# Kernel tuning notes

Hardware: AMD Instinct MI355X
Metric: run time of the kernel (lower is better)

## Reference

```python
import jax, jax.numpy as jnp
import numpy as np

N_NODES = 40000
N_EDGES = 640000
D = 128


def setup_inputs() -> dict:
    key = jax.random.key(0)
    k1, k2, k3, k4, k5 = jax.random.split(key, 5)
    x = jax.random.normal(k1, (N_NODES, D), dtype=jnp.float32)
    edge_index = jax.random.randint(k2, (2, N_EDGES), 0, N_NODES, dtype=jnp.int64)
    # torch Linear stores weight as [out, in]; xavier ~ scaled normal
    scale = (2.0 / (D + D)) ** 0.5
    W_self = jax.random.normal(k3, (D, D), dtype=jnp.float32) * scale
    W_neigh = jax.random.normal(k4, (D, D), dtype=jnp.float32) * scale
    bias = jax.random.normal(k5, (D,), dtype=jnp.float32) * 0.01
    return {"x": x, "edge_index": edge_index, "W_self": W_self,
            "W_neigh": W_neigh, "bias": bias}


def reference(x, edge_index, W_self, W_neigh, bias):
    num_nodes = x.shape[0]
    row, col = edge_index[0], edge_index[1]
    # gather source features and scatter-add into destination nodes
    agg = jax.ops.segment_sum(x[row], col, num_segments=num_nodes)  # [N, D]
    deg = jax.ops.segment_sum(jnp.ones_like(col, dtype=x.dtype), col,
                              num_segments=num_nodes)
    agg = agg / jnp.clip(deg, 1.0)[:, None]
    # h_v = lin_self(x_v) + lin_neigh(mean_u x_u) + bias  (no activation in source)
    out = x @ W_self.T + agg @ W_neigh.T + bias
    return out
```

## Files before the change

kernel.cpp:

```cpp
#include <hip/hip_runtime.h>

#define N_NODES 40000
#define N_EDGES 640000
#define D 128
#define KCAT 256
#define CAP 64
#define NXCD 8
#define PART 5000

typedef __attribute__((ext_vector_type(8))) short short8v;
typedef __attribute__((ext_vector_type(4))) float f32x4;
typedef __attribute__((ext_vector_type(2))) float f32x2;


__device__ inline unsigned short f2bf(float f) {
  union { float f; unsigned int u; } v{f};
  unsigned int r = (v.u + 0x7FFFu + ((v.u >> 16) & 1u)) >> 16;
  return (unsigned short)r;
}

__global__ __launch_bounds__(256) void prep_count_kernel(
    const float* __restrict__ x, const float* __restrict__ Ws,
    const float* __restrict__ Wn, const int* __restrict__ ei,
    unsigned short* __restrict__ Wcat, unsigned int* __restrict__ x8,
    int* __restrict__ deg, unsigned short* __restrict__ slot) {
  int b = blockIdx.x;
  int t = threadIdx.x;
  int tid = b * 256 + t;
  {
    float4 v = *reinterpret_cast<const float4*>(x + (size_t)tid * 4);
    unsigned int u = __builtin_amdgcn_cvt_pk_fp8_f32(v.x, v.y, 0, false);
    u = __builtin_amdgcn_cvt_pk_fp8_f32(v.z, v.w, u, true);
    x8[tid] = u;
  }
  if (tid < 8192) {
    int j = tid >> 6;
    int kq = tid & 63;
    int k0 = kq * 4;
    float4 v = (kq < 32)
        ? *reinterpret_cast<const float4*>(Ws + j * D + k0)
        : *reinterpret_cast<const float4*>(Wn + j * D + (k0 - D));
    ushort4 h;
    h.x = f2bf(v.x); h.y = f2bf(v.y); h.z = f2bf(v.z); h.w = f2bf(v.w);
    *reinterpret_cast<ushort4*>(Wcat + j * KCAT + k0) = h;
  }
  {
    int p = b & (NXCD - 1);
    int chunk = b >> 3;
    int lo = p * PART;
    int q = chunk * 256 + t;
    int4 r = reinterpret_cast<const int4*>(ei)[q];
    int4 c = reinterpret_cast<const int4*>(ei + N_EDGES)[q];
    if ((unsigned)(c.x - lo) < PART)
      slot[(size_t)c.x * CAP + atomicAdd(&deg[c.x], 1)] = (unsigned short)r.x;
    if ((unsigned)(c.y - lo) < PART)
      slot[(size_t)c.y * CAP + atomicAdd(&deg[c.y], 1)] = (unsigned short)r.y;
    if ((unsigned)(c.z - lo) < PART)
      slot[(size_t)c.z * CAP + atomicAdd(&deg[c.z], 1)] = (unsigned short)r.z;
    if ((unsigned)(c.w - lo) < PART)
      slot[(size_t)c.w * CAP + atomicAdd(&deg[c.w], 1)] = (unsigned short)r.w;
  }
}

__global__ __launch_bounds__(256) void gather_kernel(
    const unsigned int* __restrict__ x8, unsigned short* __restrict__ aggb,
    const int* __restrict__ deg, const unsigned short* __restrict__ slot) {
  int node = blockIdx.x * 8 + (threadIdx.x >> 5);
  int l = threadIdx.x & 31;
  int nd = deg[node];
  const unsigned short* sp = slot + (size_t)node * CAP;
  float a0 = 0.f, a1 = 0.f, a2 = 0.f, a3 = 0.f;
  int e = 0;
  for (; e + 8 <= nd; e += 8) {
    unsigned int v[8];
#pragma unroll
    for (int j = 0; j < 8; ++j) v[j] = x8[(size_t)sp[e + j] * 32 + l];
#pragma unroll
    for (int j = 0; j < 8; ++j) {
      f32x2 lo = __builtin_amdgcn_cvt_pk_f32_fp8(v[j], false);
      f32x2 hi = __builtin_amdgcn_cvt_pk_f32_fp8(v[j], true);
      a0 += lo.x; a1 += lo.y; a2 += hi.x; a3 += hi.y;
    }
  }
  for (; e + 4 <= nd; e += 4) {
    unsigned int v[4];
#pragma unroll
    for (int j = 0; j < 4; ++j) v[j] = x8[(size_t)sp[e + j] * 32 + l];
#pragma unroll
    for (int j = 0; j < 4; ++j) {
      f32x2 lo = __builtin_amdgcn_cvt_pk_f32_fp8(v[j], false);
      f32x2 hi = __builtin_amdgcn_cvt_pk_f32_fp8(v[j], true);
      a0 += lo.x; a1 += lo.y; a2 += hi.x; a3 += hi.y;
    }
  }
  for (; e < nd; ++e) {
    unsigned int v = x8[(size_t)sp[e] * 32 + l];
    f32x2 lo = __builtin_amdgcn_cvt_pk_f32_fp8(v, false);
    f32x2 hi = __builtin_amdgcn_cvt_pk_f32_fp8(v, true);
    a0 += lo.x; a1 += lo.y; a2 += hi.x; a3 += hi.y;
  }
  float inv = 1.0f / fmaxf((float)nd, 1.0f);
  ushort4 h;
  h.x = f2bf(a0 * inv); h.y = f2bf(a1 * inv);
  h.z = f2bf(a2 * inv); h.w = f2bf(a3 * inv);
  *reinterpret_cast<ushort4*>(aggb + (size_t)node * D + l * 4) = h;
}

__global__ __launch_bounds__(256) void sage_gemm_kernel(
    const float* __restrict__ x, const unsigned short* __restrict__ aggb,
    const unsigned short* __restrict__ Wcat, const float* __restrict__ bias,
    float* __restrict__ out) {
  __shared__ __align__(16) char Abuf[64 * 512];
  const int t = threadIdx.x;
  const int wave = t >> 6;
  const int lane = t & 63;
  const int node0 = blockIdx.x * 64;

  short8v breg[2][8];
#pragma unroll
  for (int jg = 0; jg < 2; ++jg) {
    int col = wave * 32 + jg * 16 + (lane & 15);
#pragma unroll
    for (int ks = 0; ks < 8; ++ks) {
      int k0 = ks * 32 + (lane >> 4) * 8;
      breg[jg][ks] =
          *reinterpret_cast<const short8v*>(Wcat + (size_t)col * KCAT + k0);
    }
  }

#pragma unroll
  for (int i = 0; i < 4; ++i) {
    int q = i * 256 + t;
    int row = q >> 4;
    int s = q & 15;
    const float* xp = x + (size_t)(node0 + row) * D + s * 8;
    float4 v0 = *reinterpret_cast<const float4*>(xp);
    float4 v1 = *reinterpret_cast<const float4*>(xp + 4);
    ushort4 h0, h1;
    h0.x = f2bf(v0.x); h0.y = f2bf(v0.y); h0.z = f2bf(v0.z); h0.w = f2bf(v0.w);
    h1.x = f2bf(v1.x); h1.y = f2bf(v1.y); h1.z = f2bf(v1.z); h1.w = f2bf(v1.w);
    char* dst = Abuf + row * 512 + ((s ^ (row & 7)) << 4);
    *reinterpret_cast<ushort4*>(dst) = h0;
    *reinterpret_cast<ushort4*>(dst + 8) = h1;
  }
#pragma unroll
  for (int i = 0; i < 4; ++i) {
    int q = i * 256 + t;
    int row = q >> 4;
    int s = 16 + (q & 15);
    int4 v = *reinterpret_cast<const int4*>(aggb + (size_t)(node0 + row) * D +
                                            (q & 15) * 8);
    *reinterpret_cast<int4*>(Abuf + row * 512 + ((s ^ (row & 7)) << 4)) = v;
  }
  __syncthreads();

  const int srow = lane & 15;
  const int c7 = lane & 7;
  const int sb = lane >> 4;

  f32x4 acc[4][2] = {};
#pragma unroll
  for (int ks = 0; ks < 8; ++ks) {
    short8v af[4];
#pragma unroll
    for (int mf = 0; mf < 4; ++mf) {
      int row = mf * 16 + srow;
      int sl = (ks * 4 + sb) ^ c7;
      af[mf] = *reinterpret_cast<const short8v*>(Abuf + row * 512 + (sl << 4));
    }
#pragma unroll
    for (int mf = 0; mf < 4; ++mf)
#pragma unroll
      for (int jg = 0; jg < 2; ++jg)
        acc[mf][jg] = __builtin_amdgcn_mfma_f32_16x16x32_bf16(
            af[mf], breg[jg][ks], acc[mf][jg], 0, 0, 0);
  }

#pragma unroll
  for (int jg = 0; jg < 2; ++jg) {
    int col = wave * 32 + jg * 16 + (lane & 15);
    float bv = bias[col];
#pragma unroll
    for (int mf = 0; mf < 4; ++mf) {
      int rbase = node0 + mf * 16 + (lane >> 4) * 4;
#pragma unroll
      for (int r = 0; r < 4; ++r) {
        out[(size_t)(rbase + r) * D + col] = acc[mf][jg][r] + bv;
      }
    }
  }
}

extern "C" void kernel_launch(void* const* d_in, const int* in_sizes, int n_in,
                              void* d_out, int out_size, void* d_ws, size_t ws_size,
                              hipStream_t stream) {
  const float* x    = (const float*)d_in[0];
  const int*   ei   = (const int*)d_in[1];
  const float* Ws   = (const float*)d_in[2];
  const float* Wn   = (const float*)d_in[3];
  const float* bias = (const float*)d_in[4];
  float* out = (float*)d_out;

  unsigned short* Wcat = (unsigned short*)d_ws;
  int* deg = (int*)(Wcat + 128 * KCAT);
  unsigned short* slot = (unsigned short*)(deg + N_NODES);
  unsigned int* x8 =
      (unsigned int*)(slot + (size_t)N_NODES * CAP);
  unsigned short* aggb =
      (unsigned short*)(x8 + (size_t)N_NODES * 32);

  hipMemsetAsync(deg, 0, N_NODES * sizeof(int), stream);
  prep_count_kernel<<<5000, 256, 0, stream>>>(x, Ws, Wn, ei, Wcat, x8, deg,
                                              slot);
  gather_kernel<<<5000, 256, 0, stream>>>(x8, aggb, deg, slot);
  sage_gemm_kernel<<<625, 256, 0, stream>>>(x, aggb, Wcat, bias, out);
}
```

Measured before the change: 70.68 us.

## Partition edges via shared-memory buckets and fuse neighbor gather into GEMM

The edge scan is restructured: each of 625 blocks reads its edges once, bins them by destination partition in LDS, and writes them to per-partition lists. A new bucket kernel then fills the CSR-like slot arrays from those lists, instead of 5000 blocks each rereading all edges and filtering. The separate gather kernel and the bf16 agg buffer are removed, and the mean aggregation now runs inside the GEMM kernel straight into LDS, two nodes interleaved per half-wave. This trades one extra launch for less edge re-reading and less agg traffic, but the GEMM now uses only 625 blocks to do the latency-bound gather, so there is less parallelism to hide that latency.

```diff
diff --git a/kernel.cpp b/kernel.cpp
--- a/kernel.cpp
+++ b/kernel.cpp
@@ -7,6 +7,8 @@
 #define CAP 64
 #define NXCD 8
 #define PART 5000
+#define PLCAP 84000
+#define CCAP 224
 
 typedef __attribute__((ext_vector_type(8))) short short8v;
 typedef __attribute__((ext_vector_type(4))) float f32x4;
@@ -19,11 +21,18 @@
   return (unsigned short)r;
 }
 
-__global__ __launch_bounds__(256) void prep_count_kernel(
+__device__ inline void acc4(unsigned int v, float& a0, float& a1, float& a2,
+                            float& a3) {
+  f32x2 lo = __builtin_amdgcn_cvt_pk_f32_fp8(v, false);
+  f32x2 hi = __builtin_amdgcn_cvt_pk_f32_fp8(v, true);
+  a0 += lo.x; a1 += lo.y; a2 += hi.x; a3 += hi.y;
+}
+
+__global__ __launch_bounds__(256) void prep_kernel(
     const float* __restrict__ x, const float* __restrict__ Ws,
     const float* __restrict__ Wn, const int* __restrict__ ei,
     unsigned short* __restrict__ Wcat, unsigned int* __restrict__ x8,
-    int* __restrict__ deg, unsigned short* __restrict__ slot) {
+    unsigned int* __restrict__ plist, int* __restrict__ pcur) {
   int b = blockIdx.x;
   int t = threadIdx.x;
   int tid = b * 256 + t;
@@ -44,70 +53,69 @@
     h.x = f2bf(v.x); h.y = f2bf(v.y); h.z = f2bf(v.z); h.w = f2bf(v.w);
     *reinterpret_cast<ushort4*>(Wcat + j * KCAT + k0) = h;
   }
-  {
-    int p = b & (NXCD - 1);
-    int chunk = b >> 3;
-    int lo = p * PART;
-    int q = chunk * 256 + t;
+  __shared__ int lcnt[NXCD];
+  __shared__ int lbase[NXCD];
+  __shared__ unsigned int lbuf[NXCD][CCAP];
+  if (b < 625) {
+    if (t < NXCD) lcnt[t] = 0;
+    __syncthreads();
+    int q = b * 256 + t;
     int4 r = reinterpret_cast<const int4*>(ei)[q];
     int4 c = reinterpret_cast<const int4*>(ei + N_EDGES)[q];
-    if ((unsigned)(c.x - lo) < PART)
-      slot[(size_t)c.x * CAP + atomicAdd(&deg[c.x], 1)] = (unsigned short)r.x;
-    if ((unsigned)(c.y - lo) < PART)
-      slot[(size_t)c.y * CAP + atomicAdd(&deg[c.y], 1)] = (unsigned short)r.y;
-    if ((unsigned)(c.z - lo) < PART)
-      slot[(size_t)c.z * CAP + atomicAdd(&deg[c.z], 1)] = (unsigned short)r.z;
-    if ((unsigned)(c.w - lo) < PART)
-      slot[(size_t)c.w * CAP + atomicAdd(&deg[c.w], 1)] = (unsigned short)r.w;
-  }
-}
-
-__global__ __launch_bounds__(256) void gather_kernel(
-    const unsigned int* __restrict__ x8, unsigned short* __restrict__ aggb,
-    const int* __restrict__ deg, const unsigned short* __restrict__ slot) {
-  int node = blockIdx.x * 8 + (threadIdx.x >> 5);
-  int l = threadIdx.x & 31;
-  int nd = deg[node];
-  const unsigned short* sp = slot + (size_t)node * CAP;
-  float a0 = 0.f, a1 = 0.f, a2 = 0.f, a3 = 0.f;
-  int e = 0;
-  for (; e + 8 <= nd; e += 8) {
-    unsigned int v[8];
-#pragma unroll
-    for (int j = 0; j < 8; ++j) v[j] = x8[(size_t)sp[e + j] * 32 + l];
-#pragma unroll
-    for (int j = 0; j < 8; ++j) {
-      f32x2 lo = __builtin_amdgcn_cvt_pk_f32_fp8(v[j], false);
-      f32x2 hi = __builtin_amdgcn_cvt_pk_f32_fp8(v[j], true);
-      a0 += lo.x; a1 += lo.y; a2 += hi.x; a3 += hi.y;
-    }
-  }
-  for (; e + 4 <= nd; e += 4) {
-    unsigned int v[4];
-#pragma unroll
-    for (int j = 0; j < 4; ++j) v[j] = x8[(size_t)sp[e + j] * 32 + l];
-#pragma unroll
-    for (int j = 0; j < 4; ++j) {
-      f32x2 lo = __builtin_amdgcn_cvt_pk_f32_fp8(v[j], false);
-      f32x2 hi = __builtin_amdgcn_cvt_pk_f32_fp8(v[j], true);
-      a0 += lo.x; a1 += lo.y; a2 += hi.x; a3 += hi.y;
-    }
-  }
-  for (; e < nd; ++e) {
-    unsigned int v = x8[(size_t)sp[e] * 32 + l];
-    f32x2 lo = __builtin_amdgcn_cvt_pk_f32_fp8(v, false);
-    f32x2 hi = __builtin_amdgcn_cvt_pk_f32_fp8(v, true);
-    a0 += lo.x; a1 += lo.y; a2 += hi.x; a3 += hi.y;
-  }
-  float inv = 1.0f / fmaxf((float)nd, 1.0f);
-  ushort4 h;
-  h.x = f2bf(a0 * inv); h.y = f2bf(a1 * inv);
-  h.z = f2bf(a2 * inv); h.w = f2bf(a3 * inv);
-  *reinterpret_cast<ushort4*>(aggb + (size_t)node * D + l * 4) = h;
+    {
+      int p = c.x / PART;
+      lbuf[p][atomicAdd(&lcnt[p], 1)] =
+          (unsigned)(c.x - p * PART) | ((unsigned)r.x << 13);
+    }
+    {
+      int p = c.y / PART;
+      lbuf[p][atomicAdd(&lcnt[p], 1)] =
+          (unsigned)(c.y - p * PART) | ((unsigned)r.y << 13);
+    }
+    {
+      int p = c.z / PART;
+      lbuf[p][atomicAdd(&lcnt[p], 1)] =
+          (unsigned)(c.z - p * PART) | ((unsigned)r.z << 13);
+    }
+    {
+      int p = c.w / PART;
+      lbuf[p][atomicAdd(&lcnt[p], 1)] =
+          (unsigned)(c.w - p * PART) | ((unsigned)r.w << 13);
+    }
+    __syncthreads();
+    if (t < NXCD) lbase[t] = atomicAdd(&pcur[t], lcnt[t]);
+    __syncthreads();
+#pragma unroll
+    for (int p = 0; p < NXCD; ++p)
+      for (int i = t; i < lcnt[p]; i += 256)
+        plist[(size_t)p * PLCAP + lbase[p] + i] = lbuf[p][i];
+  }
+}
+
+__global__ __launch_bounds__(256) void bucket_kernel(
+    const unsigned int* __restrict__ plist, const int* __restrict__ pcur,
+    int* __restrict__ deg, unsigned short* __restrict__ slot) {
+  int b = blockIdx.x;
+  int t = threadIdx.x;
+  int p = b & (NXCD - 1);
+  int idx = b >> 3;
+  int n = pcur[p];
+  int chunk = (n + 312) / 313;
+  int start = idx * chunk;
+  int end = min(n, start + chunk);
+  const unsigned int* lp = plist + (size_t)p * PLCAP;
+  int base = p * PART;
+  for (int i = start + t; i < end; i += 256) {
+    unsigned int e = lp[i];
+    int c = base + (int)(e & 0x1FFFu);
+    unsigned short r = (unsigned short)(e >> 13);
+    slot[(size_t)c * CAP + atomicAdd(&deg[c], 1)] = r;
+  }
 }
 
 __global__ __launch_bounds__(256) void sage_gemm_kernel(
-    const float* __restrict__ x, const unsigned short* __restrict__ aggb,
+    const float* __restrict__ x, const unsigned int* __restrict__ x8,
+    const int* __restrict__ deg, const unsigned short* __restrict__ slot,
     const unsigned short* __restrict__ Wcat, const float* __restrict__ bias,
     float* __restrict__ out) {
   __shared__ __align__(16) char Abuf[64 * 512];
@@ -143,14 +151,86 @@
     *reinterpret_cast<ushort4*>(dst) = h0;
     *reinterpret_cast<ushort4*>(dst + 8) = h1;
   }
-#pragma unroll
-  for (int i = 0; i < 4; ++i) {
-    int q = i * 256 + t;
-    int row = q >> 4;
-    int s = 16 + (q & 15);
-    int4 v = *reinterpret_cast<const int4*>(aggb + (size_t)(node0 + row) * D +
-                                            (q & 15) * 8);
-    *reinterpret_cast<int4*>(Abuf + row * 512 + ((s ^ (row & 7)) << 4)) = v;
+
+  {
+    int hw = t >> 5;
+    int l = t & 31;
+#pragma unroll
+    for (int pr = 0; pr < 4; ++pr) {
+      int i0 = hw * 8 + pr * 2;
+      int n0 = node0 + i0;
+      int nd0 = deg[n0], nd1 = deg[n0 + 1];
+      const unsigned short* sp0 = slot + (size_t)n0 * CAP;
+      const unsigned short* sp1 = sp0 + CAP;
+      float a00 = 0.f, a01 = 0.f, a02 = 0.f, a03 = 0.f;
+      float a10 = 0.f, a11 = 0.f, a12 = 0.f, a13 = 0.f;
+      int m = (nd0 < nd1 ? nd0 : nd1) & ~7;
+      int e = 0;
+      for (; e < m; e += 8) {
+        unsigned int v0[8], v1[8];
+#pragma unroll
+        for (int j = 0; j < 8; ++j) v0[j] = x8[(size_t)sp0[e + j] * 32 + l];
+#pragma unroll
+        for (int j = 0; j < 8; ++j) v1[j] = x8[(size_t)sp1[e + j] * 32 + l];
+#pragma unroll
+        for (int j = 0; j < 8; ++j) acc4(v0[j], a00, a01, a02, a03);
+#pragma unroll
+        for (int j = 0; j < 8; ++j) acc4(v1[j], a10, a11, a12, a13);
+      }
+      int e0 = e;
+      for (; e0 + 8 <= nd0; e0 += 8) {
+        unsigned int v[8];
+#pragma unroll
+        for (int j = 0; j < 8; ++j) v[j] = x8[(size_t)sp0[e0 + j] * 32 + l];
+#pragma unroll
+        for (int j = 0; j < 8; ++j) acc4(v[j], a00, a01, a02, a03);
+      }
+      for (; e0 + 4 <= nd0; e0 += 4) {
+        unsigned int v[4];
+#pragma unroll
+        for (int j = 0; j < 4; ++j) v[j] = x8[(size_t)sp0[e0 + j] * 32 + l];
+#pragma unroll
+        for (int j = 0; j < 4; ++j) acc4(v[j], a00, a01, a02, a03);
+      }
+      for (; e0 < nd0; ++e0) acc4(x8[(size_t)sp0[e0] * 32 + l], a00, a01, a02, a03);
+      int e1 = e;
+      for (; e1 + 8 <= nd1; e1 += 8) {
+        unsigned int v[8];
+#pragma unroll
+        for (int j = 0; j < 8; ++j) v[j] = x8[(size_t)sp1[e1 + j] * 32 + l];
+#pragma unroll
+        for (int j = 0; j < 8; ++j) acc4(v[j], a10, a11, a12, a13);
+      }
+      for (; e1 + 4 <= nd1; e1 += 4) {
+        unsigned int v[4];
+#pragma unroll
+        for (int j = 0; j < 4; ++j) v[j] = x8[(size_t)sp1[e1 + j] * 32 + l];
+#pragma unroll
+        for (int j = 0; j < 4; ++j) acc4(v[j], a10, a11, a12, a13);
+      }
+      for (; e1 < nd1; ++e1) acc4(x8[(size_t)sp1[e1] * 32 + l], a10, a11, a12, a13);
+
+      int s = 16 + (l >> 1);
+      int off = (l & 1) << 3;
+      {
+        float inv = 1.0f / fmaxf((float)nd0, 1.0f);
+        ushort4 h;
+        h.x = f2bf(a00 * inv); h.y = f2bf(a01 * inv);
+        h.z = f2bf(a02 * inv); h.w = f2bf(a03 * inv);
+        int row = i0;
+        *reinterpret_cast<ushort4*>(
+            Abuf + row * 512 + ((s ^ (row & 7)) << 4) + off) = h;
+      }
+      {
+        float inv = 1.0f / fmaxf((float)nd1, 1.0f);
+        ushort4 h;
+        h.x = f2bf(a10 * inv); h.y = f2bf(a11 * inv);
+        h.z = f2bf(a12 * inv); h.w = f2bf(a13 * inv);
+        int row = i0 + 1;
+        *reinterpret_cast<ushort4*>(
+            Abuf + row * 512 + ((s ^ (row & 7)) << 4) + off) = h;
+      }
+    }
   }
   __syncthreads();
 
@@ -203,15 +283,14 @@
 
   unsigned short* Wcat = (unsigned short*)d_ws;
   int* deg = (int*)(Wcat + 128 * KCAT);
-  unsigned short* slot = (unsigned short*)(deg + N_NODES);
+  int* pcur = deg + N_NODES;
+  unsigned short* slot = (unsigned short*)(pcur + NXCD);
   unsigned int* x8 =
       (unsigned int*)(slot + (size_t)N_NODES * CAP);
-  unsigned short* aggb =
-      (unsigned short*)(x8 + (size_t)N_NODES * 32);
-
-  hipMemsetAsync(deg, 0, N_NODES * sizeof(int), stream);
-  prep_count_kernel<<<5000, 256, 0, stream>>>(x, Ws, Wn, ei, Wcat, x8, deg,
-                                              slot);
-  gather_kernel<<<5000, 256, 0, stream>>>(x8, aggb, deg, slot);
-  sage_gemm_kernel<<<625, 256, 0, stream>>>(x, aggb, Wcat, bias, out);
-}
+  unsigned int* plist = x8 + (size_t)N_NODES * 32;
+
+  hipMemsetAsync(deg, 0, (N_NODES + NXCD) * sizeof(int), stream);
+  prep_kernel<<<5000, 256, 0, stream>>>(x, Ws, Wn, ei, Wcat, x8, plist, pcur);
+  bucket_kernel<<<2504, 256, 0, stream>>>(plist, pcur, deg, slot);
+  sage_gemm_kernel<<<625, 256, 0, stream>>>(x, x8, deg, slot, Wcat, bias, out);
+}
```

After: 103.6 us. 1.47x slower.

## Two-pass partitioned edge bucketing via shared-memory binning before slot scatter

Applied to the files above, without the earlier changes.

Edge scattering now happens in two passes instead of having each of the 5000 blocks read all edges and filter by a partition. First, 625 blocks bin edges by destination partition in shared memory and append packed (dst, src) words to per-partition lists with one global atomic per partition per block. Then a new bucket kernel processes each partition's list to fill the per-node slots. This removes the 8x redundant reading of the edge index and keeps slot atomics partition-local. The cost is an extra kernel launch and the plist round trip; plist reuses the aggb buffer and relies on fixed capacities (PLCAP, CCAP) that assume a uniform edge distribution.

```diff
diff --git a/kernel.cpp b/kernel.cpp
--- a/kernel.cpp
+++ b/kernel.cpp
@@ -7,6 +7,8 @@
 #define CAP 64
 #define NXCD 8
 #define PART 5000
+#define PLCAP 84000
+#define CCAP 224
 
 typedef __attribute__((ext_vector_type(8))) short short8v;
 typedef __attribute__((ext_vector_type(4))) float f32x4;
@@ -19,11 +21,18 @@
   return (unsigned short)r;
 }
 
-__global__ __launch_bounds__(256) void prep_count_kernel(
+__device__ inline void acc4(unsigned int v, float& a0, float& a1, float& a2,
+                            float& a3) {
+  f32x2 lo = __builtin_amdgcn_cvt_pk_f32_fp8(v, false);
+  f32x2 hi = __builtin_amdgcn_cvt_pk_f32_fp8(v, true);
+  a0 += lo.x; a1 += lo.y; a2 += hi.x; a3 += hi.y;
+}
+
+__global__ __launch_bounds__(256) void prep_kernel(
     const float* __restrict__ x, const float* __restrict__ Ws,
     const float* __restrict__ Wn, const int* __restrict__ ei,
     unsigned short* __restrict__ Wcat, unsigned int* __restrict__ x8,
-    int* __restrict__ deg, unsigned short* __restrict__ slot) {
+    unsigned int* __restrict__ plist, int* __restrict__ pcur) {
   int b = blockIdx.x;
   int t = threadIdx.x;
   int tid = b * 256 + t;
@@ -44,21 +53,63 @@
     h.x = f2bf(v.x); h.y = f2bf(v.y); h.z = f2bf(v.z); h.w = f2bf(v.w);
     *reinterpret_cast<ushort4*>(Wcat + j * KCAT + k0) = h;
   }
-  {
-    int p = b & (NXCD - 1);
-    int chunk = b >> 3;
-    int lo = p * PART;
-    int q = chunk * 256 + t;
+  __shared__ int lcnt[NXCD];
+  __shared__ int lbase[NXCD];
+  __shared__ unsigned int lbuf[NXCD][CCAP];
+  if (b < 625) {
+    if (t < NXCD) lcnt[t] = 0;
+    __syncthreads();
+    int q = b * 256 + t;
     int4 r = reinterpret_cast<const int4*>(ei)[q];
     int4 c = reinterpret_cast<const int4*>(ei + N_EDGES)[q];
-    if ((unsigned)(c.x - lo) < PART)
-      slot[(size_t)c.x * CAP + atomicAdd(&deg[c.x], 1)] = (unsigned short)r.x;
-    if ((unsigned)(c.y - lo) < PART)
-      slot[(size_t)c.y * CAP + atomicAdd(&deg[c.y], 1)] = (unsigned short)r.y;
-    if ((unsigned)(c.z - lo) < PART)
-      slot[(size_t)c.z * CAP + atomicAdd(&deg[c.z], 1)] = (unsigned short)r.z;
-    if ((unsigned)(c.w - lo) < PART)
-      slot[(size_t)c.w * CAP + atomicAdd(&deg[c.w], 1)] = (unsigned short)r.w;
+    {
+      int p = c.x / PART;
+      lbuf[p][atomicAdd(&lcnt[p], 1)] =
+          (unsigned)(c.x - p * PART) | ((unsigned)r.x << 13);
+    }
+    {
+      int p = c.y / PART;
+      lbuf[p][atomicAdd(&lcnt[p], 1)] =
+          (unsigned)(c.y - p * PART) | ((unsigned)r.y << 13);
+    }
+    {
+      int p = c.z / PART;
+      lbuf[p][atomicAdd(&lcnt[p], 1)] =
+          (unsigned)(c.z - p * PART) | ((unsigned)r.z << 13);
+    }
+    {
+      int p = c.w / PART;
+      lbuf[p][atomicAdd(&lcnt[p], 1)] =
+          (unsigned)(c.w - p * PART) | ((unsigned)r.w << 13);
+    }
+    __syncthreads();
+    if (t < NXCD) lbase[t] = atomicAdd(&pcur[t], lcnt[t]);
+    __syncthreads();
+#pragma unroll
+    for (int p = 0; p < NXCD; ++p)
+      for (int i = t; i < lcnt[p]; i += 256)
+        plist[(size_t)p * PLCAP + lbase[p] + i] = lbuf[p][i];
+  }
+}
+
+__global__ __launch_bounds__(256) void bucket_kernel(
+    const unsigned int* __restrict__ plist, const int* __restrict__ pcur,
+    int* __restrict__ deg, unsigned short* __restrict__ slot) {
+  int b = blockIdx.x;
+  int t = threadIdx.x;
+  int p = b & (NXCD - 1);
+  int idx = b >> 3;
+  int n = pcur[p];
+  int chunk = (n + 312) / 313;
+  int start = idx * chunk;
+  int end = min(n, start + chunk);
+  const unsigned int* lp = plist + (size_t)p * PLCAP;
+  int base = p * PART;
+  for (int i = start + t; i < end; i += 256) {
+    unsigned int e = lp[i];
+    int c = base + (int)(e & 0x1FFFu);
+    unsigned short r = (unsigned short)(e >> 13);
+    slot[(size_t)c * CAP + atomicAdd(&deg[c], 1)] = r;
   }
 }
 
@@ -76,29 +127,16 @@
 #pragma unroll
     for (int j = 0; j < 8; ++j) v[j] = x8[(size_t)sp[e + j] * 32 + l];
 #pragma unroll
-    for (int j = 0; j < 8; ++j) {
-      f32x2 lo = __builtin_amdgcn_cvt_pk_f32_fp8(v[j], false);
-      f32x2 hi = __builtin_amdgcn_cvt_pk_f32_fp8(v[j], true);
-      a0 += lo.x; a1 += lo.y; a2 += hi.x; a3 += hi.y;
-    }
+    for (int j = 0; j < 8; ++j) acc4(v[j], a0, a1, a2, a3);
   }
   for (; e + 4 <= nd; e += 4) {
     unsigned int v[4];
 #pragma unroll
     for (int j = 0; j < 4; ++j) v[j] = x8[(size_t)sp[e + j] * 32 + l];
 #pragma unroll
-    for (int j = 0; j < 4; ++j) {
-      f32x2 lo = __builtin_amdgcn_cvt_pk_f32_fp8(v[j], false);
-      f32x2 hi = __builtin_amdgcn_cvt_pk_f32_fp8(v[j], true);
-      a0 += lo.x; a1 += lo.y; a2 += hi.x; a3 += hi.y;
-    }
-  }
-  for (; e < nd; ++e) {
-    unsigned int v = x8[(size_t)sp[e] * 32 + l];
-    f32x2 lo = __builtin_amdgcn_cvt_pk_f32_fp8(v, false);
-    f32x2 hi = __builtin_amdgcn_cvt_pk_f32_fp8(v, true);
-    a0 += lo.x; a1 += lo.y; a2 += hi.x; a3 += hi.y;
-  }
+    for (int j = 0; j < 4; ++j) acc4(v[j], a0, a1, a2, a3);
+  }
+  for (; e < nd; ++e) acc4(x8[(size_t)sp[e] * 32 + l], a0, a1, a2, a3);
   float inv = 1.0f / fmaxf((float)nd, 1.0f);
   ushort4 h;
   h.x = f2bf(a0 * inv); h.y = f2bf(a1 * inv);
@@ -203,15 +241,17 @@
 
   unsigned short* Wcat = (unsigned short*)d_ws;
   int* deg = (int*)(Wcat + 128 * KCAT);
-  unsigned short* slot = (unsigned short*)(deg + N_NODES);
+  int* pcur = deg + N_NODES;
+  unsigned short* slot = (unsigned short*)(pcur + NXCD);
   unsigned int* x8 =
       (unsigned int*)(slot + (size_t)N_NODES * CAP);
-  unsigned short* aggb =
-      (unsigned short*)(x8 + (size_t)N_NODES * 32);
-
-  hipMemsetAsync(deg, 0, N_NODES * sizeof(int), stream);
-  prep_count_kernel<<<5000, 256, 0, stream>>>(x, Ws, Wn, ei, Wcat, x8, deg,
-                                              slot);
+  void* scratch = (void*)(x8 + (size_t)N_NODES * 32);
+  unsigned int* plist = (unsigned int*)scratch;
+  unsigned short* aggb = (unsigned short*)scratch;
+
+  hipMemsetAsync(deg, 0, (N_NODES + NXCD) * sizeof(int), stream);
+  prep_kernel<<<5000, 256, 0, stream>>>(x, Ws, Wn, ei, Wcat, x8, plist, pcur);
+  bucket_kernel<<<2504, 256, 0, stream>>>(plist, pcur, deg, slot);
   gather_kernel<<<5000, 256, 0, stream>>>(x8, aggb, deg, slot);
   sage_gemm_kernel<<<625, 256, 0, stream>>>(x, aggb, Wcat, bias, out);
 }
```

New measurement: 79.39 us. 1.12x slower.

## Fuse neighbor gather into GEMM kernel, halve tile rows, stream weights per k-step

Applied to the files above, without the earlier changes.

The separate gather kernel is removed. The GEMM kernel now computes each node's mean neighbor aggregate directly into shared memory, so the bf16 agg buffer no longer goes through global memory and one launch disappears. The GEMM tile shrinks from 64 to 32 rows, which doubles the grid to 1250 blocks. Weight fragments are now loaded from global or L2 at every k-step instead of being preloaded into registers, trading weight reloads for lower register pressure. Gather parallelism per block drops, since each half-wave now handles four nodes in sequence, which could expose latency.

```diff
diff --git a/kernel.cpp b/kernel.cpp
--- a/kernel.cpp
+++ b/kernel.cpp
@@ -19,7 +19,14 @@
   return (unsigned short)r;
 }
 
-__global__ __launch_bounds__(256) void prep_count_kernel(
+__device__ inline void acc4(unsigned int v, float& a0, float& a1, float& a2,
+                            float& a3) {
+  f32x2 lo = __builtin_amdgcn_cvt_pk_f32_fp8(v, false);
+  f32x2 hi = __builtin_amdgcn_cvt_pk_f32_fp8(v, true);
+  a0 += lo.x; a1 += lo.y; a2 += hi.x; a3 += hi.y;
+}
+
+__global__ __launch_bounds__(256) void prep_kernel(
     const float* __restrict__ x, const float* __restrict__ Ws,
     const float* __restrict__ Wn, const int* __restrict__ ei,
     unsigned short* __restrict__ Wcat, unsigned int* __restrict__ x8,
@@ -62,74 +69,19 @@
   }
 }
 
-__global__ __launch_bounds__(256) void gather_kernel(
-    const unsigned int* __restrict__ x8, unsigned short* __restrict__ aggb,
-    const int* __restrict__ deg, const unsigned short* __restrict__ slot) {
-  int node = blockIdx.x * 8 + (threadIdx.x >> 5);
-  int l = threadIdx.x & 31;
-  int nd = deg[node];
-  const unsigned short* sp = slot + (size_t)node * CAP;
-  float a0 = 0.f, a1 = 0.f, a2 = 0.f, a3 = 0.f;
-  int e = 0;
-  for (; e + 8 <= nd; e += 8) {
-    unsigned int v[8];
-#pragma unroll
-    for (int j = 0; j < 8; ++j) v[j] = x8[(size_t)sp[e + j] * 32 + l];
-#pragma unroll
-    for (int j = 0; j < 8; ++j) {
-      f32x2 lo = __builtin_amdgcn_cvt_pk_f32_fp8(v[j], false);
-      f32x2 hi = __builtin_amdgcn_cvt_pk_f32_fp8(v[j], true);
-      a0 += lo.x; a1 += lo.y; a2 += hi.x; a3 += hi.y;
-    }
-  }
-  for (; e + 4 <= nd; e += 4) {
-    unsigned int v[4];
-#pragma unroll
-    for (int j = 0; j < 4; ++j) v[j] = x8[(size_t)sp[e + j] * 32 + l];
-#pragma unroll
-    for (int j = 0; j < 4; ++j) {
-      f32x2 lo = __builtin_amdgcn_cvt_pk_f32_fp8(v[j], false);
-      f32x2 hi = __builtin_amdgcn_cvt_pk_f32_fp8(v[j], true);
-      a0 += lo.x; a1 += lo.y; a2 += hi.x; a3 += hi.y;
-    }
-  }
-  for (; e < nd; ++e) {
-    unsigned int v = x8[(size_t)sp[e] * 32 + l];
-    f32x2 lo = __builtin_amdgcn_cvt_pk_f32_fp8(v, false);
-    f32x2 hi = __builtin_amdgcn_cvt_pk_f32_fp8(v, true);
-    a0 += lo.x; a1 += lo.y; a2 += hi.x; a3 += hi.y;
-  }
-  float inv = 1.0f / fmaxf((float)nd, 1.0f);
-  ushort4 h;
-  h.x = f2bf(a0 * inv); h.y = f2bf(a1 * inv);
-  h.z = f2bf(a2 * inv); h.w = f2bf(a3 * inv);
-  *reinterpret_cast<ushort4*>(aggb + (size_t)node * D + l * 4) = h;
-}
-
 __global__ __launch_bounds__(256) void sage_gemm_kernel(
-    const float* __restrict__ x, const unsigned short* __restrict__ aggb,
+    const float* __restrict__ x, const unsigned int* __restrict__ x8,
+    const int* __restrict__ deg, const unsigned short* __restrict__ slot,
     const unsigned short* __restrict__ Wcat, const float* __restrict__ bias,
     float* __restrict__ out) {
-  __shared__ __align__(16) char Abuf[64 * 512];
+  __shared__ __align__(16) char Abuf[32 * 512];
   const int t = threadIdx.x;
   const int wave = t >> 6;
   const int lane = t & 63;
-  const int node0 = blockIdx.x * 64;
-
-  short8v breg[2][8];
-#pragma unroll
-  for (int jg = 0; jg < 2; ++jg) {
-    int col = wave * 32 + jg * 16 + (lane & 15);
-#pragma unroll
-    for (int ks = 0; ks < 8; ++ks) {
-      int k0 = ks * 32 + (lane >> 4) * 8;
-      breg[jg][ks] =
-          *reinterpret_cast<const short8v*>(Wcat + (size_t)col * KCAT + k0);
-    }
-  }
-
-#pragma unroll
-  for (int i = 0; i < 4; ++i) {
+  const int node0 = blockIdx.x * 32;
+
+#pragma unroll
+  for (int i = 0; i < 2; ++i) {
     int q = i * 256 + t;
     int row = q >> 4;
     int s = q & 15;
@@ -143,14 +95,42 @@
     *reinterpret_cast<ushort4*>(dst) = h0;
     *reinterpret_cast<ushort4*>(dst + 8) = h1;
   }
-#pragma unroll
-  for (int i = 0; i < 4; ++i) {
-    int q = i * 256 + t;
-    int row = q >> 4;
-    int s = 16 + (q & 15);
-    int4 v = *reinterpret_cast<const int4*>(aggb + (size_t)(node0 + row) * D +
-                                            (q & 15) * 8);
-    *reinterpret_cast<int4*>(Abuf + row * 512 + ((s ^ (row & 7)) << 4)) = v;
+
+  {
+    int hw = t >> 5;
+    int l = t & 31;
+#pragma unroll
+    for (int pr = 0; pr < 4; ++pr) {
+      int row = hw * 4 + pr;
+      int node = node0 + row;
+      int nd = deg[node];
+      const unsigned short* sp = slot + (size_t)node * CAP;
+      float a0 = 0.f, a1 = 0.f, a2 = 0.f, a3 = 0.f;
+      int e = 0;
+      for (; e + 8 <= nd; e += 8) {
+        unsigned int v[8];
+#pragma unroll
+        for (int j = 0; j < 8; ++j) v[j] = x8[(size_t)sp[e + j] * 32 + l];
+#pragma unroll
+        for (int j = 0; j < 8; ++j) acc4(v[j], a0, a1, a2, a3);
+      }
+      for (; e + 4 <= nd; e += 4) {
+        unsigned int v[4];
+#pragma unroll
+        for (int j = 0; j < 4; ++j) v[j] = x8[(size_t)sp[e + j] * 32 + l];
+#pragma unroll
+        for (int j = 0; j < 4; ++j) acc4(v[j], a0, a1, a2, a3);
+      }
+      for (; e < nd; ++e) acc4(x8[(size_t)sp[e] * 32 + l], a0, a1, a2, a3);
+      float inv = 1.0f / fmaxf((float)nd, 1.0f);
+      ushort4 h;
+      h.x = f2bf(a0 * inv); h.y = f2bf(a1 * inv);
+      h.z = f2bf(a2 * inv); h.w = f2bf(a3 * inv);
+      int s = 16 + (l >> 1);
+      int off = (l & 1) << 3;
+      *reinterpret_cast<ushort4*>(
+          Abuf + row * 512 + ((s ^ (row & 7)) << 4) + off) = h;
+    }
   }
   __syncthreads();
 
@@ -158,22 +138,29 @@
   const int c7 = lane & 7;
   const int sb = lane >> 4;
 
-  f32x4 acc[4][2] = {};
+  f32x4 acc[2][2] = {};
 #pragma unroll
   for (int ks = 0; ks < 8; ++ks) {
-    short8v af[4];
-#pragma unroll
-    for (int mf = 0; mf < 4; ++mf) {
+    short8v af[2];
+#pragma unroll
+    for (int mf = 0; mf < 2; ++mf) {
       int row = mf * 16 + srow;
       int sl = (ks * 4 + sb) ^ c7;
       af[mf] = *reinterpret_cast<const short8v*>(Abuf + row * 512 + (sl << 4));
     }
-#pragma unroll
-    for (int mf = 0; mf < 4; ++mf)
+    short8v bf[2];
+#pragma unroll
+    for (int jg = 0; jg < 2; ++jg) {
+      int col = wave * 32 + jg * 16 + (lane & 15);
+      bf[jg] = *reinterpret_cast<const short8v*>(Wcat + (size_t)col * KCAT +
+                                                 ks * 32 + sb * 8);
+    }
+#pragma unroll
+    for (int mf = 0; mf < 2; ++mf)
 #pragma unroll
       for (int jg = 0; jg < 2; ++jg)
         acc[mf][jg] = __builtin_amdgcn_mfma_f32_16x16x32_bf16(
-            af[mf], breg[jg][ks], acc[mf][jg], 0, 0, 0);
+            af[mf], bf[jg], acc[mf][jg], 0, 0, 0);
   }
 
 #pragma unroll
@@ -181,7 +168,7 @@
     int col = wave * 32 + jg * 16 + (lane & 15);
     float bv = bias[col];
 #pragma unroll
-    for (int mf = 0; mf < 4; ++mf) {
+    for (int mf = 0; mf < 2; ++mf) {
       int rbase = node0 + mf * 16 + (lane >> 4) * 4;
 #pragma unroll
       for (int r = 0; r < 4; ++r) {
@@ -206,12 +193,9 @@
   unsigned short* slot = (unsigned short*)(deg + N_NODES);
   unsigned int* x8 =
       (unsigned int*)(slot + (size_t)N_NODES * CAP);
-  unsigned short* aggb =
-      (unsigned short*)(x8 + (size_t)N_NODES * 32);
 
   hipMemsetAsync(deg, 0, N_NODES * sizeof(int), stream);
-  prep_count_kernel<<<5000, 256, 0, stream>>>(x, Ws, Wn, ei, Wcat, x8, deg,
-                                              slot);
-  gather_kernel<<<5000, 256, 0, stream>>>(x8, aggb, deg, slot);
-  sage_gemm_kernel<<<625, 256, 0, stream>>>(x, aggb, Wcat, bias, out);
-}
+  prep_kernel<<<5000, 256, 0, stream>>>(x, Ws, Wn, ei, Wcat, x8, deg, slot);
+  sage_gemm_kernel<<<1250, 256, 0, stream>>>(x, x8, deg, slot, Wcat, bias,
+                                             out);
+}
```

Measured after the change: 72.23 us. +2.2%, slower.
